# Kernel optimization log

Measured on AMD Instinct MI355X. Metric: run time of the kernel, lower is better.

The kernel has to match this reference:

```python
import jax, jax.numpy as jnp
import numpy as np

N, D, E, H, TOPK = 16384, 1024, 8, 4096, 2


def setup_inputs() -> dict:
    key = jax.random.key(0)
    ks = jax.random.split(key, 7)
    s_in = 1.0 / np.sqrt(D)
    s_h = 1.0 / np.sqrt(H)
    return {
        "x": jax.random.normal(ks[0], (N, D), jnp.float32),
        "Wg": jax.random.uniform(ks[1], (D, E), jnp.float32, -s_in, s_in),
        "bg": jnp.zeros((E,), jnp.float32),
        "W1": jax.random.uniform(ks[2], (E, D, H), jnp.float32, -s_in, s_in),
        "b1": jax.random.uniform(ks[3], (E, H), jnp.float32, -s_in, s_in),
        "W2": jax.random.uniform(ks[4], (E, H, D), jnp.float32, -s_h, s_h),
        "b2": jax.random.uniform(ks[5], (E, D), jnp.float32, -s_h, s_h),
    }


def _moe_forward(x, Wg, bg, W1, b1, W2, b2):
    # Gate: softmax over experts, top-k, renormalize (standard TopKGate)
    logits = x @ Wg + bg                       # (N, E)
    probs = jax.nn.softmax(logits, axis=-1)
    gates, idxs = jax.lax.top_k(probs, TOPK)   # (N, K)
    gates = gates / jnp.sum(gates, axis=-1, keepdims=True)

    # combine weight per token per expert: cw[n,e] = sum_k gates[n,k]*[idxs[n,k]==e]
    onehot = jax.nn.one_hot(idxs, E, dtype=x.dtype)        # (N, K, E)
    cw = jnp.einsum("nk,nke->ne", gates, onehot)           # (N, E)

    # per-expert 2-layer MLP, gated combine (loop over small fixed expert set)
    out = jnp.zeros_like(x)
    for e in range(E):
        h = jax.nn.relu(x @ W1[e] + b1[e])     # (N, H)
        y = h @ W2[e] + b2[e]                  # (N, D)
        out = out + cw[:, e:e + 1] * y

    # aux loss: for each expert with >=1 routed token, add mean(gates[:,0])^2
    counts = jnp.sum(onehot, axis=(0, 1))                  # (E,)
    active = (counts > 0).astype(x.dtype)                  # (E,)
    m = jnp.mean(gates[:, 0])
    aux_loss = jnp.sum(active) * m * m
    return out, aux_loss


def reference(x, Wg, bg, W1, b1, W2, b2):
    return _moe_forward(x, Wg, bg, W1, b1, W2, b2)
```

## Files before the change

### kernel.cpp

```cpp
#include <hip/hip_runtime.h>
#include <stdint.h>

typedef unsigned short u16;
typedef __bf16 bf16x8 __attribute__((ext_vector_type(8)));
typedef float f32x4 __attribute__((ext_vector_type(4)));

#define N_TOK 16384
#define DIM   1024
#define NEXP  8
#define HID   4096
#define MT256 136
#define MT128 272
#define PADROWS 34816

__device__ __forceinline__ u16 f2bf(float f) {
  uint32_t u = __builtin_bit_cast(uint32_t, f);
  u += 0x7fffu + ((u >> 16) & 1u);
  return (u16)(u >> 16);
}

__device__ __forceinline__ float bf2f(u16 v) {
  uint32_t u = (uint32_t)v << 16;
  return __builtin_bit_cast(float, u);
}

__device__ __forceinline__ void gload16(const void* g, void* l) {
  __builtin_amdgcn_global_load_lds(
      (const __attribute__((address_space(1))) uint32_t*)g,
      (__attribute__((address_space(3))) uint32_t*)l, 16, 0, 0);
}


__global__ void k_zero(int* counts) {
  if (threadIdx.x < NEXP) counts[threadIdx.x] = 0;
}

__global__ void k_tcast(const float* __restrict__ src, u16* __restrict__ dst,
                        int R, int C) {
  __shared__ float tile[32][33];
  int nc = C >> 5, nr = R >> 5;
  int t = blockIdx.x;
  int cb = t % nc; t /= nc;
  int rb = t % nr; int ee = t / nr;
  const float* s0 = src + ((size_t)ee * R + (size_t)rb * 32) * C + cb * 32;
  int tx = threadIdx.x & 31, ty = threadIdx.x >> 5;
#pragma unroll
  for (int i = 0; i < 4; ++i)
    tile[ty + i * 8][tx] = s0[(size_t)(ty + i * 8) * C + tx];
  __syncthreads();
  u16* d0 = dst + ((size_t)ee * C + (size_t)cb * 32) * R + rb * 32;
#pragma unroll
  for (int i = 0; i < 4; ++i)
    d0[(size_t)(ty + i * 8) * R + tx] = f2bf(tile[tx][ty + i * 8]);
}


__global__ __launch_bounds__(256) void k_gate(
    const float* __restrict__ x, const float* __restrict__ Wg,
    const float* __restrict__ bg, u16* __restrict__ xb,
    int* __restrict__ tok_e, float* __restrict__ tok_g,
    float* __restrict__ blocksums) {
  __shared__ float wg_s[NEXP * DIM];
  __shared__ float s4[4];
  for (int i = threadIdx.x; i < NEXP * DIM; i += 256) {
    int k = i >> 3, e = i & 7;
    wg_s[e * DIM + k] = Wg[i];
  }
  __syncthreads();
  int lane = threadIdx.x & 63, wv = threadIdx.x >> 6;
  int n = blockIdx.x * 4 + wv;
  const float4* xr4 = (const float4*)(x + (size_t)n * DIM);
  float4 xv[4];
#pragma unroll
  for (int i = 0; i < 4; ++i) xv[i] = xr4[lane + 64 * i];
  ushort4* xo4 = (ushort4*)(xb + (size_t)n * DIM);
#pragma unroll
  for (int i = 0; i < 4; ++i) {
    ushort4 p;
    p.x = f2bf(xv[i].x); p.y = f2bf(xv[i].y);
    p.z = f2bf(xv[i].z); p.w = f2bf(xv[i].w);
    xo4[lane + 64 * i] = p;
  }
  float acc[8];
#pragma unroll
  for (int e = 0; e < 8; ++e) {
    const float4* w4 = (const float4*)(wg_s + e * DIM);
    float a = 0.f;
#pragma unroll
    for (int i = 0; i < 4; ++i) {
      float4 wv4 = w4[lane + 64 * i];
      a += xv[i].x * wv4.x + xv[i].y * wv4.y + xv[i].z * wv4.z +
           xv[i].w * wv4.w;
    }
    acc[e] = a;
  }
#pragma unroll
  for (int e = 0; e < 8; ++e)
#pragma unroll
    for (int off = 32; off > 0; off >>= 1)
      acc[e] += __shfl_xor(acc[e], off);

  if (lane == 0) {
    float l0 = -1e30f, l1 = -1e30f; int e0 = 0, e1 = 0;
#pragma unroll
    for (int e = 0; e < 8; ++e) {
      float v = acc[e] + bg[e];
      if (v > l0) { l1 = l0; e1 = e0; l0 = v; e0 = e; }
      else if (v > l1) { l1 = v; e1 = e; }
    }
    float g0 = 1.f / (1.f + expf(l1 - l0));
    float g1 = 1.f - g0;
    tok_e[2 * n] = e0; tok_e[2 * n + 1] = e1;
    tok_g[2 * n] = g0; tok_g[2 * n + 1] = g1;
    s4[wv] = g0;
  }
  __syncthreads();
  if (threadIdx.x == 0) blocksums[blockIdx.x] = s4[0] + s4[1] + s4[2] + s4[3];
}


__global__ __launch_bounds__(256) void k_hist(const int* __restrict__ tok_e,
                                              int* __restrict__ counts) {
  __shared__ int lcnt[8];
  if (threadIdx.x < 8) lcnt[threadIdx.x] = 0;
  __syncthreads();
  int base4 = (blockIdx.x * 256 + threadIdx.x) * 2;
  const int4* t4 = (const int4*)tok_e;
  int4 a = t4[base4], b = t4[base4 + 1];
  int v[8] = {a.x, a.y, a.z, a.w, b.x, b.y, b.z, b.w};
  int c[8];
#pragma unroll
  for (int ee = 0; ee < 8; ++ee) {
    int s = 0;
#pragma unroll
    for (int i = 0; i < 8; ++i) s += (v[i] == ee);
    c[ee] = s;
  }
  int lane = threadIdx.x & 63;
#pragma unroll
  for (int ee = 0; ee < 8; ++ee) {
    int s = c[ee];
#pragma unroll
    for (int off = 32; off > 0; off >>= 1) s += __shfl_xor(s, off);
    if (lane == 0 && s) atomicAdd(&lcnt[ee], s);
  }
  __syncthreads();
  if (threadIdx.x < 8 && lcnt[threadIdx.x])
    atomicAdd(&counts[threadIdx.x], lcnt[threadIdx.x]);
}


__global__ __launch_bounds__(256) void k_setup(
    const int* __restrict__ counts, const float* __restrict__ blocksums,
    int* __restrict__ padded_off, int* __restrict__ cursor,
    int* __restrict__ row2tok, float* __restrict__ aux_out) {
  __shared__ float red[256];
  __shared__ int off_s[9];
  float s = 0.f;
  for (int i = threadIdx.x; i < 4096; i += 256) s += blocksums[i];
  red[threadIdx.x] = s;
  __syncthreads();
  for (int st = 128; st > 0; st >>= 1) {
    if (threadIdx.x < st) red[threadIdx.x] += red[threadIdx.x + st];
    __syncthreads();
  }
  if (threadIdx.x == 0) {
    int off = 0, nact = 0;
    for (int e = 0; e < 8; ++e) {
      off_s[e] = off;
      int c = counts[e];
      if (c > 0) nact++;
      off += ((c + 255) >> 8) << 8;
      cursor[e] = 0;
    }
    off_s[8] = off;
    for (int e = 0; e <= 8; ++e) padded_off[e] = off_s[e];
    float m = red[0] / (float)N_TOK;
    *aux_out = (float)nact * m * m;
  }
  __syncthreads();
  for (int idx = threadIdx.x; idx < NEXP * 256; idx += 256) {
    int e = idx >> 8, i = idx & 255;
    int slot = off_s[e] + counts[e] + i;
    if (slot < off_s[e + 1]) row2tok[slot] = 0;
  }
}


__global__ __launch_bounds__(256) void k_scatter(
    int* __restrict__ tok_e, const int* __restrict__ padded_off,
    int* __restrict__ cursor, int* __restrict__ row2tok) {
  __shared__ int lcnt[8], lbase[8];
  if (threadIdx.x < 8) lcnt[threadIdx.x] = 0;
  __syncthreads();
  int n = blockIdx.x * 256 + threadIdx.x;
  int e0 = tok_e[2 * n], e1 = tok_e[2 * n + 1];
  int p0 = atomicAdd(&lcnt[e0], 1);
  int p1 = atomicAdd(&lcnt[e1], 1);
  __syncthreads();
  if (threadIdx.x < 8 && lcnt[threadIdx.x])
    lbase[threadIdx.x] = atomicAdd(&cursor[threadIdx.x], lcnt[threadIdx.x]);
  __syncthreads();
  int s0 = padded_off[e0] + lbase[e0] + p0;
  int s1 = padded_off[e1] + lbase[e1] + p1;
  row2tok[s0] = n;
  row2tok[s1] = n;
  tok_e[2 * n] = s0;
  tok_e[2 * n + 1] = s1;
}


__global__ __launch_bounds__(512, 2) void k_gemm1_8p(
    const u16* __restrict__ xb, const u16* __restrict__ w1t,
    const float* __restrict__ b1, const int* __restrict__ row2tok,
    const int* __restrict__ padded_off, u16* __restrict__ h) {
  __shared__ u16 ldsA[32768];
  __shared__ u16 ldsB[32768];
  int n0 = blockIdx.x * 256;
  int row0 = blockIdx.y * 256;
  if (row0 >= padded_off[8]) return;
  int e = 0;
  while (row0 >= padded_off[e + 1]) ++e;
  int tid = threadIdx.x, lane = tid & 63, wv = tid >> 6;
  int wm = wv >> 2, wn = wv & 3;
  int fr = lane & 15, fq = lane >> 4;
  int r = tid >> 2;
  int clog = ((tid & 3) ^ ((tid >> 3) & 3)) * 8;
  const u16* a0 = xb + (size_t)row2tok[row0 + r] * DIM + clog;
  const u16* a1 = xb + (size_t)row2tok[row0 + 128 + r] * DIM + clog;
  const u16* wp = w1t + (size_t)e * (HID * DIM);
  const u16* b0p = wp + (size_t)(n0 + r) * DIM + clog;
  const u16* b1p = wp + (size_t)(n0 + 128 + r) * DIM + clog;

  f32x4 acc[8][4];
#pragma unroll
  for (int i = 0; i < 8; ++i)
#pragma unroll
    for (int j = 0; j < 4; ++j) acc[i][j] = (f32x4){0.f, 0.f, 0.f, 0.f};
  bf16x8 av[4], bv[4];

#define ST1(ISB, T, KK, KOF)                                              \
  do {                                                                   \
    u16* d_ = ((ISB) ? ldsB : ldsA) + ((T) * 2 + (KK)) * 8192 + wv * 512; \
    gload16(((ISB) ? b0p : a0) + (KOF), d_);                             \
    gload16(((ISB) ? b1p : a1) + (KOF), d_ + 4096);                      \
  } while (0)

#define RD8(T, KK, IH, LB)                                                \
  do {                                                                   \
    const u16* Ar = ldsA + ((T) * 2 + (KK)) * 8192;                      \
    _Pragma("unroll") for (int i = 0; i < 4; ++i) {                      \
      int ar = wm * 128 + ((IH) * 4 + i) * 16 + fr;                      \
      av[i] = *(const bf16x8*)&Ar[ar * 32 + ((fq ^ ((ar >> 1) & 3)) * 8)]; \
    }                                                                    \
    if (LB) {                                                            \
      const u16* Br = ldsB + ((T) * 2 + (KK)) * 8192;                    \
      _Pragma("unroll") for (int j = 0; j < 4; ++j) {                    \
        int br = wn * 64 + j * 16 + fr;                                  \
        bv[j] = *(const bf16x8*)&Br[br * 32 + ((fq ^ ((br >> 1) & 3)) * 8)]; \
      }                                                                  \
    }                                                                    \
  } while (0)

#define PH(T, KK, IH, LB, DOST, SB, STT, SKK, SKOF, VM6, VM0)            \
  do {                                                                   \
    RD8(T, KK, IH, LB);                                                  \
    if (DOST) ST1(SB, STT, SKK, SKOF);                                   \
    if (VM6) asm volatile("s_waitcnt vmcnt(6)" ::: "memory");            \
    if (VM0) asm volatile("s_waitcnt vmcnt(0)" ::: "memory");            \
    asm volatile("s_barrier" ::: "memory");                              \
    asm volatile("s_waitcnt lgkmcnt(0)" ::: "memory");                   \
    __builtin_amdgcn_sched_barrier(0);                                   \
    __builtin_amdgcn_s_setprio(1);                                       \
    _Pragma("unroll") for (int i = 0; i < 4; ++i)                        \
      _Pragma("unroll") for (int j = 0; j < 4; ++j)                      \
        acc[(IH) * 4 + i][j] = __builtin_amdgcn_mfma_f32_16x16x32_bf16(  \
            av[i], bv[j], acc[(IH) * 4 + i][j], 0, 0, 0);                \
    __builtin_amdgcn_s_setprio(0);                                       \
    asm volatile("s_barrier" ::: "memory");                              \
  } while (0)

  ST1(1, 0, 0, 0);  ST1(0, 0, 0, 0);  ST1(1, 0, 1, 32); ST1(0, 0, 1, 32);
  ST1(1, 1, 0, 64); ST1(0, 1, 0, 64); ST1(1, 1, 1, 96);
  asm volatile("s_waitcnt vmcnt(6)" ::: "memory");
  asm volatile("s_barrier" ::: "memory");

  constexpr int NI = DIM / 128;
  for (int kt = 0; kt < NI - 1; ++kt) {
    int k0 = kt * 128;
    PH(0, 0, 0, 1, 1, 0, 1, 1, k0 + 96,  0, 0);
    PH(0, 0, 1, 0, 1, 1, 0, 0, k0 + 128, 0, 0);
    PH(0, 1, 0, 1, 1, 0, 0, 0, k0 + 128, 0, 0);
    PH(0, 1, 1, 0, 1, 1, 0, 1, k0 + 160, 1, 0);
    PH(1, 0, 0, 1, 1, 0, 0, 1, k0 + 160, 0, 0);
    PH(1, 0, 1, 0, 1, 1, 1, 0, k0 + 192, 0, 0);
    PH(1, 1, 0, 1, 1, 0, 1, 0, k0 + 192, 0, 0);
    PH(1, 1, 1, 0, 1, 1, 1, 1, k0 + 224, 1, 0);
  }
  {
    int k0 = (NI - 1) * 128;
    PH(0, 0, 0, 1, 1, 0, 1, 1, k0 + 96, 0, 0);
    PH(0, 0, 1, 0, 0, 0, 0, 0, 0, 0, 0);
    PH(0, 1, 0, 1, 0, 0, 0, 0, 0, 0, 0);
    PH(0, 1, 1, 0, 0, 0, 0, 0, 0, 0, 1);
    PH(1, 0, 0, 1, 0, 0, 0, 0, 0, 0, 0);
    PH(1, 0, 1, 0, 0, 0, 0, 0, 0, 0, 0);
    PH(1, 1, 0, 1, 0, 0, 0, 0, 0, 0, 0);
    PH(1, 1, 1, 0, 0, 0, 0, 0, 0, 0, 0);
  }
#undef PH
#undef RD8
#undef ST1

  float bv4[4];
#pragma unroll
  for (int j = 0; j < 4; ++j)
    bv4[j] = b1[e * HID + n0 + wn * 64 + j * 16 + fr];

#pragma unroll
  for (int rf = 0; rf < 8; ++rf) {
#pragma unroll
    for (int jj = 0; jj < 4; ++jj) {
      int grow = row0 + wm * 128 + rf * 16 + fq * 4 + jj;
      u16* hr = h + (size_t)grow * HID + n0 + wn * 64 + fr;
#pragma unroll
      for (int j = 0; j < 4; ++j) {
        float v = acc[rf][j][jj] + bv4[j];
        hr[j * 16] = f2bf(v > 0.f ? v : 0.f);
      }
    }
  }
}


__global__ __launch_bounds__(256, 3) void k_gemm2(
    const u16* __restrict__ hh, const u16* __restrict__ w2t,
    const float* __restrict__ b2, const int* __restrict__ padded_off,
    u16* __restrict__ y0, u16* __restrict__ y1) {
  __shared__ u16 Abuf[3][4096];
  __shared__ u16 Bbuf[3][4096];
  int d = blockIdx.x;
  int xcd = d & 7;
  int n_t = (d >> 3) & 7;
  int rg  = d >> 6;
  int row0 = (rg * 8 + xcd) * 128;
  if (row0 >= padded_off[8]) return;
  int e = 0;
  while (row0 >= padded_off[e + 1]) ++e;
  int n0 = n_t * 128;
  int tid = threadIdx.x, lane = tid & 63, wv = tid >> 6;
  int wm = wv >> 1, wn = wv & 1;
  int fr = lane & 15, fq = lane >> 4;
  int ra0 = tid >> 2, ra1 = 64 + (tid >> 2);
  int ca = (((tid & 3) ^ ((tid >> 3) & 3))) * 8;
  const u16* asrc0 = hh + (size_t)(row0 + ra0) * HID + ca;
  const u16* asrc1 = hh + (size_t)(row0 + ra1) * HID + ca;
  const u16* bb = w2t + (size_t)e * (HID * DIM);
  const u16* bsrc0 = bb + (size_t)(n0 + ra0) * HID + ca;
  const u16* bsrc1 = bb + (size_t)(n0 + ra1) * HID + ca;
  int lo = wv * 512;
  int sq = (fq ^ ((fr >> 1) & 3)) * 8;

  f32x4 acc[4][4];
#pragma unroll
  for (int i = 0; i < 4; ++i)
#pragma unroll
    for (int j = 0; j < 4; ++j) acc[i][j] = (f32x4){0.f, 0.f, 0.f, 0.f};
  bf16x8 av[4], bv[4];

#define STG(b, kt)                                 \
  do {                                             \
    int ko = (kt) * 32;                            \
    gload16(asrc0 + ko, &Abuf[b][lo]);             \
    gload16(asrc1 + ko, &Abuf[b][2048 + lo]);      \
    gload16(bsrc0 + ko, &Bbuf[b][lo]);             \
    gload16(bsrc1 + ko, &Bbuf[b][2048 + lo]);      \
  } while (0)

#define CMP(b)                                                                 \
  do {                                                                         \
    _Pragma("unroll") for (int fm = 0; fm < 4; ++fm)                           \
        av[fm] = *(const bf16x8*)&Abuf[b][(wm * 64 + fm * 16 + fr) * 32 + sq]; \
    _Pragma("unroll") for (int fn = 0; fn < 4; ++fn)                           \
        bv[fn] = *(const bf16x8*)&Bbuf[b][(wn * 64 + fn * 16 + fr) * 32 + sq]; \
    _Pragma("unroll") for (int fm = 0; fm < 4; ++fm)                           \
        _Pragma("unroll") for (int fn = 0; fn < 4; ++fn)                       \
            acc[fm][fn] = __builtin_amdgcn_mfma_f32_16x16x32_bf16(             \
                av[fm], bv[fn], acc[fm][fn], 0, 0, 0);                         \
  } while (0)

  constexpr int NK = HID / 32;
  STG(0, 0);
  STG(1, 1);
  int rb = 0;
  for (int kt = 0; kt < NK - 2; ++kt) {
    int sb = rb + 2; if (sb >= 3) sb -= 3;
    STG(sb, kt + 2);
    asm volatile("s_waitcnt vmcnt(8)" ::: "memory");
    asm volatile("s_barrier" ::: "memory");
    CMP(rb);
    asm volatile("s_waitcnt lgkmcnt(0)" ::: "memory");
    asm volatile("s_barrier" ::: "memory");
    if (++rb == 3) rb = 0;
  }
  asm volatile("s_waitcnt vmcnt(4)" ::: "memory");
  asm volatile("s_barrier" ::: "memory");
  CMP(rb);
  if (++rb == 3) rb = 0;
  asm volatile("s_waitcnt vmcnt(0)" ::: "memory");
  asm volatile("s_barrier" ::: "memory");
  CMP(rb);
#undef STG
#undef CMP

  float bv4[4];
#pragma unroll
  for (int fn = 0; fn < 4; ++fn)
    bv4[fn] = b2[e * DIM + n0 + wn * 64 + fn * 16 + fr];

#pragma unroll
  for (int fm = 0; fm < 4; ++fm) {
#pragma unroll
    for (int j = 0; j < 4; ++j) {
      int grow = row0 + wm * 64 + fm * 16 + fq * 4 + j;
      u16* ybase = grow < 16384 ? y0 + (size_t)grow * DIM
                                : y1 + (size_t)(grow - 16384) * DIM;
      u16* orow = ybase + n0 + wn * 64 + fr;
#pragma unroll
      for (int fn = 0; fn < 4; ++fn)
        orow[fn * 16] = f2bf(acc[fm][fn][j] + bv4[fn]);
    }
  }
}


__global__ __launch_bounds__(256) void k_combine(
    const u16* __restrict__ y0, const u16* __restrict__ y1,
    const int* __restrict__ slots, const float* __restrict__ tok_g,
    float* __restrict__ out) {
  int n = blockIdx.x;
  int s0 = slots[2 * n], s1 = slots[2 * n + 1];
  float g0 = tok_g[2 * n], g1 = tok_g[2 * n + 1];
  int d = threadIdx.x * 4;
  const u16* ya = (s0 < 16384 ? y0 + (size_t)s0 * DIM
                              : y1 + (size_t)(s0 - 16384) * DIM) + d;
  const u16* yb = (s1 < 16384 ? y0 + (size_t)s1 * DIM
                              : y1 + (size_t)(s1 - 16384) * DIM) + d;
  ushort4 a = *(const ushort4*)ya;
  ushort4 b = *(const ushort4*)yb;
  float4 o;
  o.x = g0 * bf2f(a.x) + g1 * bf2f(b.x);
  o.y = g0 * bf2f(a.y) + g1 * bf2f(b.y);
  o.z = g0 * bf2f(a.z) + g1 * bf2f(b.z);
  o.w = g0 * bf2f(a.w) + g1 * bf2f(b.w);
  *(float4*)(out + (size_t)n * DIM + d) = o;
}


extern "C" void kernel_launch(void* const* d_in, const int* in_sizes, int n_in,
                              void* d_out, int out_size, void* d_ws,
                              size_t ws_size, hipStream_t stream) {
  const float* x  = (const float*)d_in[0];
  const float* Wg = (const float*)d_in[1];
  const float* bg = (const float*)d_in[2];
  const float* W1 = (const float*)d_in[3];
  const float* b1 = (const float*)d_in[4];
  const float* W2 = (const float*)d_in[5];
  const float* b2 = (const float*)d_in[6];
  float* out = (float*)d_out;

  char* w = (char*)d_ws;
  u16* xb          = (u16*)(w);
  u16* y0          = (u16*)(w);
  u16* wT          = (u16*)(w + 33554432);
  u16* h           = (u16*)(w + 100663296);
  u16* y1          = (u16*)(w + 385875968);
  int* tok_e       = (int*)(w + 423624704);
  float* tok_g     = (float*)(w + 423755776);
  int* counts      = (int*)(w + 423886848);
  int* cursor      = (int*)(w + 423887104);
  int* padded_off  = (int*)(w + 423887360);
  int* row2tok     = (int*)(w + 423887616);
  float* blocksums = (float*)(w + 424026880);

  k_zero<<<1, 64, 0, stream>>>(counts);
  k_gate<<<4096, 256, 0, stream>>>(x, Wg, bg, xb, tok_e, tok_g, blocksums);
  k_hist<<<16, 256, 0, stream>>>(tok_e, counts);
  k_setup<<<1, 256, 0, stream>>>(counts, blocksums, padded_off, cursor, row2tok,
                                 out + (size_t)N_TOK * DIM);
  k_scatter<<<64, 256, 0, stream>>>(tok_e, padded_off, cursor, row2tok);
  k_tcast<<<32768, 256, 0, stream>>>(W1, wT, DIM, HID);
  k_gemm1_8p<<<dim3(HID / 256, MT256), 512, 0, stream>>>(
      xb, wT, b1, row2tok, padded_off, h);
  k_tcast<<<32768, 256, 0, stream>>>(W2, wT, HID, DIM);
  k_gemm2<<<MT128 * (DIM / 128), 256, 0, stream>>>(
      h, wT, b2, padded_off, y0, y1);
  k_combine<<<N_TOK, 256, 0, stream>>>(y0, y1, tok_e, tok_g, out);
}
```

Measured before the change: 827.0 us.

## Reuse 256x256 eight-phase GEMM kernel for second expert GEMM

Templates the first-layer 256x256-tile, 512-thread, eight-phase pipelined GEMM on K dimension and mode, and uses it for the second expert GEMM in place of the separate 128x128 triple-buffered kernel. Larger tiles raise arithmetic intensity and cut redundant loads of h and W2. The trade-off is fewer blocks for the N=1024 GEMM (4 column tiles x 136 row tiles), which may hurt occupancy and tail balance, and the XCD-aware block mapping is lost.

```diff
diff --git a/kernel.cpp b/kernel.cpp
--- a/kernel.cpp
+++ b/kernel.cpp
@@ -10,7 +10,6 @@
 #define NEXP  8
 #define HID   4096
 #define MT256 136
-#define MT128 272
 #define PADROWS 34816
 
 __device__ __forceinline__ u16 f2bf(float f) {
@@ -210,12 +209,15 @@
 }
 
 
-__global__ __launch_bounds__(512, 2) void k_gemm1_8p(
-    const u16* __restrict__ xb, const u16* __restrict__ w1t,
-    const float* __restrict__ b1, const int* __restrict__ row2tok,
-    const int* __restrict__ padded_off, u16* __restrict__ h) {
+template <int KDIM, int MODE>
+__global__ __launch_bounds__(512, 2) void k_gemm_8p(
+    const u16* __restrict__ Asrc, const u16* __restrict__ Wt,
+    const float* __restrict__ bias, const int* __restrict__ row2tok,
+    const int* __restrict__ padded_off, u16* __restrict__ out0,
+    u16* __restrict__ out1) {
   __shared__ u16 ldsA[32768];
   __shared__ u16 ldsB[32768];
+  constexpr int NDIM = MODE ? DIM : HID;
   int n0 = blockIdx.x * 256;
   int row0 = blockIdx.y * 256;
   if (row0 >= padded_off[8]) return;
@@ -226,11 +228,17 @@
   int fr = lane & 15, fq = lane >> 4;
   int r = tid >> 2;
   int clog = ((tid & 3) ^ ((tid >> 3) & 3)) * 8;
-  const u16* a0 = xb + (size_t)row2tok[row0 + r] * DIM + clog;
-  const u16* a1 = xb + (size_t)row2tok[row0 + 128 + r] * DIM + clog;
-  const u16* wp = w1t + (size_t)e * (HID * DIM);
-  const u16* b0p = wp + (size_t)(n0 + r) * DIM + clog;
-  const u16* b1p = wp + (size_t)(n0 + 128 + r) * DIM + clog;
+  const u16 *a0, *a1;
+  if (MODE == 0) {
+    a0 = Asrc + (size_t)row2tok[row0 + r] * KDIM + clog;
+    a1 = Asrc + (size_t)row2tok[row0 + 128 + r] * KDIM + clog;
+  } else {
+    a0 = Asrc + (size_t)(row0 + r) * KDIM + clog;
+    a1 = Asrc + (size_t)(row0 + 128 + r) * KDIM + clog;
+  }
+  const u16* wp = Wt + (size_t)e * (HID * DIM);
+  const u16* b0p = wp + (size_t)(n0 + r) * KDIM + clog;
+  const u16* b1p = wp + (size_t)(n0 + 128 + r) * KDIM + clog;
 
   f32x4 acc[8][4];
 #pragma unroll
@@ -285,7 +293,7 @@
   asm volatile("s_waitcnt vmcnt(6)" ::: "memory");
   asm volatile("s_barrier" ::: "memory");
 
-  constexpr int NI = DIM / 128;
+  constexpr int NI = KDIM / 128;
   for (int kt = 0; kt < NI - 1; ++kt) {
     int k0 = kt * 128;
     PH(0, 0, 0, 1, 1, 0, 1, 1, k0 + 96,  0, 0);
@@ -315,120 +323,27 @@
   float bv4[4];
 #pragma unroll
   for (int j = 0; j < 4; ++j)
-    bv4[j] = b1[e * HID + n0 + wn * 64 + j * 16 + fr];
+    bv4[j] = bias[e * NDIM + n0 + wn * 64 + j * 16 + fr];
 
 #pragma unroll
   for (int rf = 0; rf < 8; ++rf) {
 #pragma unroll
     for (int jj = 0; jj < 4; ++jj) {
       int grow = row0 + wm * 128 + rf * 16 + fq * 4 + jj;
-      u16* hr = h + (size_t)grow * HID + n0 + wn * 64 + fr;
+      u16* orow;
+      if (MODE == 0) {
+        orow = out0 + (size_t)grow * NDIM + n0 + wn * 64 + fr;
+      } else {
+        orow = (grow < 16384 ? out0 + (size_t)grow * NDIM
+                             : out1 + (size_t)(grow - 16384) * NDIM) +
+               n0 + wn * 64 + fr;
+      }
 #pragma unroll
       for (int j = 0; j < 4; ++j) {
         float v = acc[rf][j][jj] + bv4[j];
-        hr[j * 16] = f2bf(v > 0.f ? v : 0.f);
+        if (MODE == 0) v = v > 0.f ? v : 0.f;
+        orow[j * 16] = f2bf(v);
       }
-    }
-  }
-}
-
-
-__global__ __launch_bounds__(256, 3) void k_gemm2(
-    const u16* __restrict__ hh, const u16* __restrict__ w2t,
-    const float* __restrict__ b2, const int* __restrict__ padded_off,
-    u16* __restrict__ y0, u16* __restrict__ y1) {
-  __shared__ u16 Abuf[3][4096];
-  __shared__ u16 Bbuf[3][4096];
-  int d = blockIdx.x;
-  int xcd = d & 7;
-  int n_t = (d >> 3) & 7;
-  int rg  = d >> 6;
-  int row0 = (rg * 8 + xcd) * 128;
-  if (row0 >= padded_off[8]) return;
-  int e = 0;
-  while (row0 >= padded_off[e + 1]) ++e;
-  int n0 = n_t * 128;
-  int tid = threadIdx.x, lane = tid & 63, wv = tid >> 6;
-  int wm = wv >> 1, wn = wv & 1;
-  int fr = lane & 15, fq = lane >> 4;
-  int ra0 = tid >> 2, ra1 = 64 + (tid >> 2);
-  int ca = (((tid & 3) ^ ((tid >> 3) & 3))) * 8;
-  const u16* asrc0 = hh + (size_t)(row0 + ra0) * HID + ca;
-  const u16* asrc1 = hh + (size_t)(row0 + ra1) * HID + ca;
-  const u16* bb = w2t + (size_t)e * (HID * DIM);
-  const u16* bsrc0 = bb + (size_t)(n0 + ra0) * HID + ca;
-  const u16* bsrc1 = bb + (size_t)(n0 + ra1) * HID + ca;
-  int lo = wv * 512;
-  int sq = (fq ^ ((fr >> 1) & 3)) * 8;
-
-  f32x4 acc[4][4];
-#pragma unroll
-  for (int i = 0; i < 4; ++i)
-#pragma unroll
-    for (int j = 0; j < 4; ++j) acc[i][j] = (f32x4){0.f, 0.f, 0.f, 0.f};
-  bf16x8 av[4], bv[4];
-
-#define STG(b, kt)                                 \
-  do {                                             \
-    int ko = (kt) * 32;                            \
-    gload16(asrc0 + ko, &Abuf[b][lo]);             \
-    gload16(asrc1 + ko, &Abuf[b][2048 + lo]);      \
-    gload16(bsrc0 + ko, &Bbuf[b][lo]);             \
-    gload16(bsrc1 + ko, &Bbuf[b][2048 + lo]);      \
-  } while (0)
-
-#define CMP(b)                                                                 \
-  do {                                                                         \
-    _Pragma("unroll") for (int fm = 0; fm < 4; ++fm)                           \
-        av[fm] = *(const bf16x8*)&Abuf[b][(wm * 64 + fm * 16 + fr) * 32 + sq]; \
-    _Pragma("unroll") for (int fn = 0; fn < 4; ++fn)                           \
-        bv[fn] = *(const bf16x8*)&Bbuf[b][(wn * 64 + fn * 16 + fr) * 32 + sq]; \
-    _Pragma("unroll") for (int fm = 0; fm < 4; ++fm)                           \
-        _Pragma("unroll") for (int fn = 0; fn < 4; ++fn)                       \
-            acc[fm][fn] = __builtin_amdgcn_mfma_f32_16x16x32_bf16(             \
-                av[fm], bv[fn], acc[fm][fn], 0, 0, 0);                         \
-  } while (0)
-
-  constexpr int NK = HID / 32;
-  STG(0, 0);
-  STG(1, 1);
-  int rb = 0;
-  for (int kt = 0; kt < NK - 2; ++kt) {
-    int sb = rb + 2; if (sb >= 3) sb -= 3;
-    STG(sb, kt + 2);
-    asm volatile("s_waitcnt vmcnt(8)" ::: "memory");
-    asm volatile("s_barrier" ::: "memory");
-    CMP(rb);
-    asm volatile("s_waitcnt lgkmcnt(0)" ::: "memory");
-    asm volatile("s_barrier" ::: "memory");
-    if (++rb == 3) rb = 0;
-  }
-  asm volatile("s_waitcnt vmcnt(4)" ::: "memory");
-  asm volatile("s_barrier" ::: "memory");
-  CMP(rb);
-  if (++rb == 3) rb = 0;
-  asm volatile("s_waitcnt vmcnt(0)" ::: "memory");
-  asm volatile("s_barrier" ::: "memory");
-  CMP(rb);
-#undef STG
-#undef CMP
-
-  float bv4[4];
-#pragma unroll
-  for (int fn = 0; fn < 4; ++fn)
-    bv4[fn] = b2[e * DIM + n0 + wn * 64 + fn * 16 + fr];
-
-#pragma unroll
-  for (int fm = 0; fm < 4; ++fm) {
-#pragma unroll
-    for (int j = 0; j < 4; ++j) {
-      int grow = row0 + wm * 64 + fm * 16 + fq * 4 + j;
-      u16* ybase = grow < 16384 ? y0 + (size_t)grow * DIM
-                                : y1 + (size_t)(grow - 16384) * DIM;
-      u16* orow = ybase + n0 + wn * 64 + fr;
-#pragma unroll
-      for (int fn = 0; fn < 4; ++fn)
-        orow[fn * 16] = f2bf(acc[fm][fn][j] + bv4[fn]);
     }
   }
 }
@@ -490,10 +405,10 @@
                                  out + (size_t)N_TOK * DIM);
   k_scatter<<<64, 256, 0, stream>>>(tok_e, padded_off, cursor, row2tok);
   k_tcast<<<32768, 256, 0, stream>>>(W1, wT, DIM, HID);
-  k_gemm1_8p<<<dim3(HID / 256, MT256), 512, 0, stream>>>(
-      xb, wT, b1, row2tok, padded_off, h);
+  k_gemm_8p<DIM, 0><<<dim3(HID / 256, MT256), 512, 0, stream>>>(
+      xb, wT, b1, row2tok, padded_off, h, nullptr);
   k_tcast<<<32768, 256, 0, stream>>>(W2, wT, HID, DIM);
-  k_gemm2<<<MT128 * (DIM / 128), 256, 0, stream>>>(
-      h, wT, b2, padded_off, y0, y1);
+  k_gemm_8p<HID, 1><<<dim3(DIM / 256, MT256), 512, 0, stream>>>(
+      h, wT, b2, row2tok, padded_off, y0, y1);
   k_combine<<<N_TOK, 256, 0, stream>>>(y0, y1, tok_e, tok_g, out);
 }
```

Result: slower. 863.6 us (+4.4%).
